# Kernel optimization log

Measured on AMD Instinct MI355X. Metric: run time of the kernel, lower is better.

## Reference

```python
import jax, jax.numpy as jnp
import numpy as np

N_ITEMS = 100001  # n_items + 1 (padding idx 0)
D = 128           # item_embedding_dim == hidden_size
P = 3             # purposes
S, B = 100, 256   # seq_len, batch
TAU = 0.1
EPS = 0.01


def setup_inputs() -> dict:
    key = jax.random.key(0)
    ks = jax.random.split(key, 6)
    std = 1.0 / np.sqrt(D)
    seq = jax.random.randint(ks[0], (S, B), 0, N_ITEMS)          # [S, B] item ids
    lens = jax.random.randint(ks[1], (B,), 1, S + 1)             # valid lengths in [1, S]
    emb_table = jax.random.uniform(ks[2], (N_ITEMS, D), minval=-std, maxval=std, dtype=jnp.float32)
    purpose_table = jax.random.uniform(ks[3], (P, D), minval=-std, maxval=std, dtype=jnp.float32)
    x2h_w = jax.random.uniform(ks[4], (P, 3 * D, D), minval=-std, maxval=std, dtype=jnp.float32)  # 3 cells
    h2h_w = jax.random.uniform(ks[5], (P, 3 * D, D), minval=-std, maxval=std, dtype=jnp.float32)
    return {"seq": seq, "lens": lens, "emb_table": emb_table,
            "purpose_table": purpose_table, "x2h_w": x2h_w, "h2h_w": h2h_w}


def _psru_cell(x, h, concen, Wx, Wh):
    # x: [B,D], h: [B,D], concen: [B], Wx/Wh: [3D, D]
    gx = x @ Wx.T                              # [B, 3D]
    gh = h @ Wh.T                              # [B, 3D]
    i_r, i_i, i_n = jnp.split(gx, 3, axis=1)
    h_r, h_i, h_n = jnp.split(gh, 3, axis=1)
    resetgate = jax.nn.sigmoid(i_r + h_r)
    inputgate = jax.nn.sigmoid(i_i + h_i)
    newgate = jnp.tanh(i_n + resetgate * h_n)
    multi = jnp.where(concen >= EPS, concen, 0.0)[:, None] * inputgate
    return h + multi * (newgate - h)


def reference(seq, lens, emb_table, purpose_table, x2h_w, h2h_w):
    # padding_idx = 0
    emb_table = emb_table.at[0].set(0.0)
    # concentration matrix: softmax over purposes of normalized-embedding similarity / tau
    item_n = emb_table / jnp.clip(jnp.linalg.norm(emb_table, axis=1, keepdims=True), 1e-12)
    attr_n = purpose_table / jnp.clip(jnp.linalg.norm(purpose_table, axis=1, keepdims=True), 1e-12)
    g = jax.nn.softmax((item_n @ attr_n.T) / TAU, axis=1)   # [V, P]  (exp/sum == softmax)
    g = g.at[0].set(0.0)

    embs = emb_table[seq]        # [S, B, D]
    g_seq = g[seq]               # [S, B, P]

    h0 = jnp.zeros((P, B, D), emb_table.dtype)

    def step(h, xs):
        x, gq = xs  # x: [B,D], gq: [B,P]
        h_new = jnp.stack([_psru_cell(x, h[p], gq[:, p], x2h_w[p], h2h_w[p]) for p in range(P)])
        return h_new, h_new

    _, hs = jax.lax.scan(step, h0, (embs, g_seq))            # hs: [S, P, B, D]

    # select hidden at last valid step per example: outs[lens-1, arange(B)]
    h_last = hs[lens - 1, :, jnp.arange(B), :]               # [B, P, D]

    # delta_c[b,v] = sum_p g[v,p] * <h_last[b,p], item_n[v]>  (== original VC_cand * item_embs sum)
    logits = sum((h_last[:, p, :] @ item_n.T) * g[None, :, p] for p in range(P))  # [B, V]
    return jax.nn.sigmoid(logits)
```

## Files before the change

kernel.cpp:

```cpp
#include <hip/hip_runtime.h>
#include <hip/hip_bf16.h>
#include <math.h>

#define N_ITEMS 100001
#define DIM 128
#define NP 3
#define SEQ 100
#define NB 256
#define G3 384
#define TAU 0.1f
#define EPS_C 0.01f

#define OFF_G     0
#define OFF_C     300016
#define OFF_WXT   600032
#define OFF_WHT   747488
#define OFF_HLAST 894944
#define OFF_GX    993248
#define WS_FLOATS_PATHA (993248 + 29491200)

typedef float f32x4 __attribute__((ext_vector_type(4)));
typedef short s16x8 __attribute__((ext_vector_type(8)));
typedef unsigned int u32x4 __attribute__((ext_vector_type(4)));
typedef _Float16 f16x8 __attribute__((ext_vector_type(8)));
typedef __fp16 hf16x2 __attribute__((ext_vector_type(2)));

__device__ __forceinline__ float sigmoidf_fast(float x) {
    return __builtin_amdgcn_rcpf(1.f + __builtin_amdgcn_exp2f(-1.4426950408889634f * x));
}
__device__ __forceinline__ float tanhf_fast(float x) {
    return 1.f - 2.f * __builtin_amdgcn_rcpf(1.f + __builtin_amdgcn_exp2f(2.8853900817779268f * x));
}
__device__ __forceinline__ unsigned short f2bf(float x) {
    union { float f; unsigned u; } v; v.f = x;
    unsigned r = v.u + 0x7fffu + ((v.u >> 16) & 1u);
    return (unsigned short)(r >> 16);
}
__device__ __forceinline__ float bf2f(unsigned short h) {
    union { unsigned u; float f; } v; v.u = ((unsigned)h) << 16;
    return v.f;
}
__device__ __forceinline__ unsigned cvt_pk_bf16(float a, float b) {
    unsigned r;
    asm("v_cvt_pk_bf16_f32 %0, %1, %2" : "=v"(r) : "v"(a), "v"(b));
    return r;
}
__device__ __forceinline__ f32x4 mfma16(s16x8 a, s16x8 b, f32x4 c) {
    return __builtin_amdgcn_mfma_f32_16x16x32_f16(
        __builtin_bit_cast(f16x8, a), __builtin_bit_cast(f16x8, b), c, 0, 0, 0);
}

__global__ void k_prep_w(const float* __restrict__ x2h, const float* __restrict__ h2h,
                         float* __restrict__ wxT, float* __restrict__ whT) {
    int idx = blockIdx.x * 256 + threadIdx.x;
    if (idx >= NP * DIM * G3) return;
    int j = idx % G3;
    int k = (idx / G3) % DIM;
    int p = idx / (G3 * DIM);
    wxT[idx] = x2h[((size_t)p * G3 + j) * DIM + k];
    whT[idx] = h2h[((size_t)p * G3 + j) * DIM + k];
}

__global__ __launch_bounds__(256) void k_prep_wA(const float* __restrict__ x2h,
                                                 const float* __restrict__ h2h,
                                                 short* __restrict__ wxA_hi,
                                                 short* __restrict__ wxA_lo,
                                                 short* __restrict__ whA_hi,
                                                 short* __restrict__ whA_lo) {
    int e = blockIdx.x * 256 + threadIdx.x;
    if (e >= 2 * NP * 24 * 4 * 64) return;
    int which = (e >= NP * 24 * 4 * 64);
    int f = which ? e - NP * 24 * 4 * 64 : e;
    const float* tab = which ? h2h : x2h;
    short* dh = which ? whA_hi : wxA_hi;
    short* dl = which ? whA_lo : wxA_lo;
    int lane = f & 63;
    int ks = (f >> 6) & 3;
    int mt = (f >> 8) % 24;
    int p  = f / 6144;
    int j = mt * 16 + (lane & 15);
    int d = ks * 32 + (lane >> 4) * 8;
    const float* src = tab + ((size_t)p * G3 + j) * DIM + d;
    short hi[8], lo[8];
    if (which) {
#pragma unroll
        for (int u = 0; u < 8; ++u) {
            float x = src[u];
            _Float16 hf = (_Float16)x;
            _Float16 lf = (_Float16)((x - (float)hf) * 2048.f);
            hi[u] = __builtin_bit_cast(short, hf);
            lo[u] = __builtin_bit_cast(short, lf);
        }
    } else {
#pragma unroll
        for (int u = 0; u < 8; ++u) {
            float x = src[u];
            unsigned short h = f2bf(x);
            hi[u] = (short)h;
            lo[u] = (short)f2bf(x - bf2f(h));
        }
    }
    *(s16x8*)(dh + (size_t)f * 8) = *(const s16x8*)hi;
    *(s16x8*)(dl + (size_t)f * 8) = *(const s16x8*)lo;
}

__global__ __launch_bounds__(256) void k_gc(const float* __restrict__ emb,
                                            const float* __restrict__ pt,
                                            float* __restrict__ g, float* __restrict__ c) {
    __shared__ float pt_l[G3];
    __shared__ float ainv[NP];
    int tid = threadIdx.x;
    for (int u = tid; u < G3; u += 256) pt_l[u] = pt[u];
    __syncthreads();
    if (tid < NP) {
        float ss = 0.f;
        for (int k = 0; k < DIM; ++k) { float v = pt_l[tid * DIM + k]; ss += v * v; }
        ainv[tid] = 1.f / fmaxf(sqrtf(ss), 1e-12f);
    }
    __syncthreads();
    int lane = tid & 63, wv = tid >> 6;
    for (int it = 0; it < 8; ++it) {
        int i = blockIdx.x * 32 + wv * 8 + it;
        if (i >= N_ITEMS) continue;
        float a = emb[(size_t)i * DIM + lane];
        float b = emb[(size_t)i * DIM + 64 + lane];
        float ss = a * a + b * b;
        float d0 = a * pt_l[lane]       + b * pt_l[64 + lane];
        float d1 = a * pt_l[128 + lane] + b * pt_l[192 + lane];
        float d2 = a * pt_l[256 + lane] + b * pt_l[320 + lane];
        for (int off = 32; off > 0; off >>= 1) {
            ss += __shfl_down(ss, off);
            d0 += __shfl_down(d0, off);
            d1 += __shfl_down(d1, off);
            d2 += __shfl_down(d2, off);
        }
        if (lane == 0) {
            if (i == 0) {
                g[0] = 0.f; g[1] = 0.f; g[2] = 0.f;
                c[0] = 0.f; c[1] = 0.f; c[2] = 0.f;
            } else {
                float inv = 1.f / fmaxf(sqrtf(ss), 1e-12f);
                float l0 = d0 * ainv[0] * inv * (1.f / TAU);
                float l1 = d1 * ainv[1] * inv * (1.f / TAU);
                float l2 = d2 * ainv[2] * inv * (1.f / TAU);
                float m = fmaxf(l0, fmaxf(l1, l2));
                float e0 = expf(l0 - m), e1 = expf(l1 - m), e2 = expf(l2 - m);
                float is = 1.f / (e0 + e1 + e2);
                float g0 = e0 * is, g1 = e1 * is, g2 = e2 * is;
                g[(size_t)i * 3 + 0] = g0; g[(size_t)i * 3 + 1] = g1; g[(size_t)i * 3 + 2] = g2;
                c[(size_t)i * 3 + 0] = g0 * inv; c[(size_t)i * 3 + 1] = g1 * inv; c[(size_t)i * 3 + 2] = g2 * inv;
            }
        }
    }
}

__global__ __launch_bounds__(512, 2) void k_gx_mfma(const int* __restrict__ seq,
                                                    const float* __restrict__ emb,
                                                    const short* __restrict__ wxA_hi,
                                                    const short* __restrict__ wxA_lo,
                                                    float* __restrict__ gx) {
    int bid = blockIdx.x;
    int t  = bid >> 4;
    int b0 = (bid & 15) * 16;
    int tid = threadIdx.x;
    int lane = tid & 63;
    int w = tid >> 6;
    int n = lane & 15;
    int q = lane >> 4;

    __shared__ int idx_l[16];
    __shared__ __align__(16) unsigned short xH[2048];
    __shared__ __align__(16) unsigned short xL[2048];

    if (tid < 16) idx_l[tid] = seq[t * NB + b0 + tid];
    __syncthreads();

    {
        int tk = tid >> 5, s = tid & 31;
        float4 v = *(const float4*)(emb + (size_t)idx_l[tk] * DIM + s * 4);
        int k = s * 4;
        int ks = k >> 5, km = k & 31;
        int ln = (km >> 3) * 16 + tk;
        int j0 = km & 7;
        int o = ks * 512 + ln * 8 + j0;
        float xv[4] = {v.x, v.y, v.z, v.w};
        unsigned short sh[4], sl[4];
#pragma unroll
        for (int r = 0; r < 4; ++r) {
            sh[r] = f2bf(xv[r]);
            sl[r] = f2bf(xv[r] - bf2f(sh[r]));
        }
        *(uint2*)(xH + o) = make_uint2((unsigned)sh[0] | ((unsigned)sh[1] << 16),
                                       (unsigned)sh[2] | ((unsigned)sh[3] << 16));
        *(uint2*)(xL + o) = make_uint2((unsigned)sl[0] | ((unsigned)sl[1] << 16),
                                       (unsigned)sl[2] | ((unsigned)sl[3] << 16));
    }
    __syncthreads();

    s16x8 bh[4], bl[4];
#pragma unroll
    for (int ks = 0; ks < 4; ++ks) {
        bh[ks] = ((const s16x8*)xH)[ks * 64 + lane];
        bl[ks] = ((const s16x8*)xL)[ks * 64 + lane];
    }

    float* gxt = gx + (size_t)(t * 3) * NB * G3;
#pragma unroll 3
    for (int ji = 0; ji < 9; ++ji) {
        int pid = w + ji * 8;
        int p = pid / 24, mt = pid % 24;
        f32x4 acc = {0.f, 0.f, 0.f, 0.f};
#pragma unroll
        for (int ks = 0; ks < 4; ++ks) {
            size_t ao = ((((size_t)p * 24 + mt) * 4 + ks) * 64 + lane) * 8;
            s16x8 ah = *(const s16x8*)(wxA_hi + ao);
            s16x8 al = *(const s16x8*)(wxA_lo + ao);
            acc = __builtin_amdgcn_mfma_f32_16x16x32_bf16(ah, bl[ks], acc, 0, 0, 0);
            acc = __builtin_amdgcn_mfma_f32_16x16x32_bf16(al, bh[ks], acc, 0, 0, 0);
            acc = __builtin_amdgcn_mfma_f32_16x16x32_bf16(ah, bh[ks], acc, 0, 0, 0);
        }
        float* o = gxt + ((size_t)p * NB + b0 + n) * G3 + mt * 16 + q * 4;
        *(float4*)o = make_float4(acc[0], acc[1], acc[2], acc[3]);
    }
}

__global__ __launch_bounds__(512, 2) void k_rnn3(const int* __restrict__ seq,
                                                 const int* __restrict__ lens,
                                                 const float* __restrict__ g,
                                                 const short* __restrict__ whA_hi,
                                                 const float* __restrict__ gx,
                                                 float* __restrict__ hlast) {
    int bid = blockIdx.x;
    int p  = bid / 16;
    int b0 = (bid % 16) * 16;
    int tid = threadIdx.x;
    int lane = tid & 63;
    int w = tid >> 6;
    int n = lane & 15;
    int q = lane >> 4;
    int d0 = w * 16 + q * 4;

    __shared__ __align__(16) unsigned short hH[2 * 2048];
    __shared__ __align__(16) unsigned short hL[2 * 2048];
    __shared__ float conc_s[SEQ * 16];

    for (int u = tid; u < 2048; u += 512) { hH[u] = 0; hL[u] = 0; }

    for (int e = tid; e < SEQ * 16; e += 512) {
        int t = e >> 4, b = e & 15;
        int ix = seq[t * NB + b0 + b];
        float cc = g[(size_t)ix * 3 + p];
        conc_s[e] = (cc >= EPS_C) ? cc : 0.f;
    }

    s16x8 whF[3][4];
    int mts0 = w, mts1 = 8 + w, mts2 = 16 + w;
#pragma unroll
    for (int ks = 0; ks < 4; ++ks) {
        size_t o0 = ((((size_t)p * 24 + mts0) * 4 + ks) * 64 + lane) * 8;
        size_t o1 = ((((size_t)p * 24 + mts1) * 4 + ks) * 64 + lane) * 8;
        size_t o2 = ((((size_t)p * 24 + mts2) * 4 + ks) * 64 + lane) * 8;
        whF[0][ks] = *(const s16x8*)(whA_hi + o0);
        whF[1][ks] = *(const s16x8*)(whA_hi + o1);
        whF[2][ks] = *(const s16x8*)(whA_hi + o2);
    }

    int len_n = lens[b0 + n];
    float h0 = 0.f, h1 = 0.f, h2 = 0.f, h3 = 0.f;

    int wks = d0 >> 5;
    int km  = d0 & 31;
    int rl  = (km >> 3) * 16 + n;
    int jj0 = km & 7;
    int widx = wks * 512 + rl * 8 + jj0;

    const float* gxbase = gx + ((size_t)p * NB + (b0 + n)) * G3 + d0;
    const size_t tstride = (size_t)3 * NB * G3;

    f32x4 pgr = *(const f32x4*)(gxbase);
    f32x4 pgi = *(const f32x4*)(gxbase + DIM);
    f32x4 pgn = *(const f32x4*)(gxbase + 2 * DIM);

    __syncthreads();

    const float SC = 4.8828125e-4f;

    int cur = 0;
    for (int t = 0; t < SEQ; ++t) {
        f32x4 grv = pgr, giv = pgi, gnv = pgn;
        int tn = (t + 1 < SEQ) ? (t + 1) : t;
        const float* gp = gxbase + (size_t)tn * tstride;
        pgr = *(const f32x4*)(gp);
        pgi = *(const f32x4*)(gp + DIM);
        pgn = *(const f32x4*)(gp + 2 * DIM);

        float cc = conc_s[t * 16 + n];

        const s16x8* bhp = (const s16x8*)hH + cur * 256 + lane;
        const s16x8* blp = (const s16x8*)hL + cur * 256 + lane;
        s16x8 bh0 = bhp[0],   bh1 = bhp[64],  bh2 = bhp[128], bh3 = bhp[192];
        s16x8 bl0 = blp[0],   bl1 = blp[64],  bl2 = blp[128], bl3 = blp[192];

        f32x4 aA0 = grv, aB0 = {0.f,0.f,0.f,0.f};
        aA0 = mfma16(whF[0][0], bh0, aA0);  aB0 = mfma16(whF[0][0], bl0, aB0);
        aA0 = mfma16(whF[0][1], bh1, aA0);  aB0 = mfma16(whF[0][1], bl1, aB0);
        aA0 = mfma16(whF[0][2], bh2, aA0);  aB0 = mfma16(whF[0][2], bl2, aB0);
        aA0 = mfma16(whF[0][3], bh3, aA0);  aB0 = mfma16(whF[0][3], bl3, aB0);
        __builtin_amdgcn_sched_barrier(0);
        float rr0 = sigmoidf_fast(fmaf(aB0[0], SC, aA0[0]));
        float rr1 = sigmoidf_fast(fmaf(aB0[1], SC, aA0[1]));
        float rr2 = sigmoidf_fast(fmaf(aB0[2], SC, aA0[2]));
        float rr3 = sigmoidf_fast(fmaf(aB0[3], SC, aA0[3]));
        __builtin_amdgcn_sched_barrier(0);
        f32x4 aA1 = giv, aB1 = {0.f,0.f,0.f,0.f};
        aA1 = mfma16(whF[1][0], bh0, aA1);  aB1 = mfma16(whF[1][0], bl0, aB1);
        aA1 = mfma16(whF[1][1], bh1, aA1);  aB1 = mfma16(whF[1][1], bl1, aB1);
        aA1 = mfma16(whF[1][2], bh2, aA1);  aB1 = mfma16(whF[1][2], bl2, aB1);
        aA1 = mfma16(whF[1][3], bh3, aA1);  aB1 = mfma16(whF[1][3], bl3, aB1);
        __builtin_amdgcn_sched_barrier(0);
        float m20 = cc * sigmoidf_fast(fmaf(aB1[0], SC, aA1[0]));
        float m21 = cc * sigmoidf_fast(fmaf(aB1[1], SC, aA1[1]));
        float m22 = cc * sigmoidf_fast(fmaf(aB1[2], SC, aA1[2]));
        float m23 = cc * sigmoidf_fast(fmaf(aB1[3], SC, aA1[3]));
        __builtin_amdgcn_sched_barrier(0);
        f32x4 aA2 = {0.f,0.f,0.f,0.f}, aB2 = {0.f,0.f,0.f,0.f};
        aA2 = mfma16(whF[2][0], bh0, aA2);  aB2 = mfma16(whF[2][0], bl0, aB2);
        aA2 = mfma16(whF[2][1], bh1, aA2);  aB2 = mfma16(whF[2][1], bl1, aB2);
        aA2 = mfma16(whF[2][2], bh2, aA2);  aB2 = mfma16(whF[2][2], bl2, aB2);
        aA2 = mfma16(whF[2][3], bh3, aA2);  aB2 = mfma16(whF[2][3], bl3, aB2);
        __builtin_amdgcn_sched_barrier(0);
        float hn0 = fmaf(aB2[0], SC, aA2[0]);
        float hn1 = fmaf(aB2[1], SC, aA2[1]);
        float hn2 = fmaf(aB2[2], SC, aA2[2]);
        float hn3 = fmaf(aB2[3], SC, aA2[3]);
        float ng0 = tanhf_fast(fmaf(rr0, hn0, gnv[0]));
        float ng1 = tanhf_fast(fmaf(rr1, hn1, gnv[1]));
        float ng2 = tanhf_fast(fmaf(rr2, hn2, gnv[2]));
        float ng3 = tanhf_fast(fmaf(rr3, hn3, gnv[3]));
        float hnew0 = fmaf(m20, ng0 - h0, h0);
        float hnew1 = fmaf(m21, ng1 - h1, h1);
        float hnew2 = fmaf(m22, ng2 - h2, h2);
        float hnew3 = fmaf(m23, ng3 - h3, h3);
        h0 = hnew0; h1 = hnew1; h2 = hnew2; h3 = hnew3;

        if (t == len_n - 1) {
            float* hp = hlast + (size_t)(b0 + n) * G3 + p * DIM + d0;
            *(float4*)hp = make_float4(h0, h1, h2, h3);
        }

        hf16x2 c01 = __builtin_amdgcn_cvt_pkrtz(hnew0, hnew1);
        hf16x2 c23 = __builtin_amdgcn_cvt_pkrtz(hnew2, hnew3);
        float e0 = (hnew0 - (float)c01[0]) * 2048.f;
        float e1 = (hnew1 - (float)c01[1]) * 2048.f;
        float e2 = (hnew2 - (float)c23[0]) * 2048.f;
        float e3 = (hnew3 - (float)c23[1]) * 2048.f;
        hf16x2 d01 = __builtin_amdgcn_cvt_pkrtz(e0, e1);
        hf16x2 d23 = __builtin_amdgcn_cvt_pkrtz(e2, e3);
        int wb = (cur ^ 1) * 2048 + widx;
        *(uint2*)(hH + wb) = make_uint2(__builtin_bit_cast(unsigned, c01),
                                        __builtin_bit_cast(unsigned, c23));
        *(uint2*)(hL + wb) = make_uint2(__builtin_bit_cast(unsigned, d01),
                                        __builtin_bit_cast(unsigned, d23));

        asm volatile("s_waitcnt lgkmcnt(0)" ::: "memory");
        __builtin_amdgcn_sched_barrier(0);
        __builtin_amdgcn_s_barrier();
        __builtin_amdgcn_sched_barrier(0);
        cur ^= 1;
    }
}

__global__ __launch_bounds__(384) void k_rnn(const int* __restrict__ seq,
                                             const int* __restrict__ lens,
                                             const float* __restrict__ emb,
                                             const float* __restrict__ g,
                                             const float* __restrict__ wxT,
                                             const float* __restrict__ whT,
                                             float* __restrict__ hlast) {
    int bid = blockIdx.x;
    int b0 = (bid & 63) * 4;
    int p = bid >> 6;
    __shared__ __align__(16) float h_l[DIM * 4];
    __shared__ __align__(16) float x_l[DIM * 4];
    __shared__ __align__(16) float sx_l[G3 * 4];
    __shared__ __align__(16) float sh_l[G3 * 4];
    __shared__ float conc_l[4];
    __shared__ int idx_l[4];
    __shared__ int len_l[4];
    int tid = threadIdx.x;
    if (tid < 4) len_l[tid] = lens[b0 + tid];
    for (int u = tid; u < DIM * 4; u += 384) h_l[u] = 0.f;
    __syncthreads();
    const float* wh = whT + (size_t)p * (DIM * G3);
    const float* wx = wxT + (size_t)p * (DIM * G3);
    for (int t = 0; t < SEQ; ++t) {
        if (tid < 4) {
            int ix = seq[t * NB + b0 + tid];
            idx_l[tid] = ix;
            conc_l[tid] = g[(size_t)ix * 3 + p];
        }
        __syncthreads();
        for (int u = tid; u < DIM * 4; u += 384) {
            int bc = u >> 7, k = u & 127;
            x_l[k * 4 + bc] = emb[(size_t)idx_l[bc] * DIM + k];
        }
        __syncthreads();
        int j = tid;
        float ax0 = 0.f, ax1 = 0.f, ax2 = 0.f, ax3 = 0.f;
#pragma unroll 4
        for (int k = 0; k < DIM; ++k) {
            float wv = wx[(size_t)k * G3 + j];
            float4 xv = *(const float4*)(x_l + k * 4);
            ax0 += wv * xv.x; ax1 += wv * xv.y; ax2 += wv * xv.z; ax3 += wv * xv.w;
        }
        float ah0 = 0.f, ah1 = 0.f, ah2 = 0.f, ah3 = 0.f;
#pragma unroll 4
        for (int k = 0; k < DIM; ++k) {
            float wv = wh[(size_t)k * G3 + j];
            float4 hv = *(const float4*)(h_l + k * 4);
            ah0 += wv * hv.x; ah1 += wv * hv.y; ah2 += wv * hv.z; ah3 += wv * hv.w;
        }
        *(float4*)(sx_l + j * 4) = make_float4(ax0, ax1, ax2, ax3);
        *(float4*)(sh_l + j * 4) = make_float4(ah0, ah1, ah2, ah3);
        __syncthreads();
        for (int u = tid; u < DIM * 4; u += 384) {
            int bc = u & 3, d = u >> 2;
            float sr = sx_l[d * 4 + bc] + sh_l[d * 4 + bc];
            float si = sx_l[(DIM + d) * 4 + bc] + sh_l[(DIM + d) * 4 + bc];
            float xn = sx_l[(2 * DIM + d) * 4 + bc];
            float hn = sh_l[(2 * DIM + d) * 4 + bc];
            float r  = sigmoidf_fast(sr);
            float ig = sigmoidf_fast(si);
            float ng = tanhf_fast(xn + r * hn);
            float h  = h_l[d * 4 + bc];
            float cc = conc_l[bc];
            float multi = (cc >= EPS_C ? cc : 0.f) * ig;
            float hnew = h + multi * (ng - h);
            h_l[d * 4 + bc] = hnew;
            if (t == len_l[bc] - 1)
                hlast[(size_t)(b0 + bc) * G3 + p * DIM + d] = hnew;
        }
        __syncthreads();
    }
}

__global__ __launch_bounds__(256) void k_prep_h(const float* __restrict__ hlast,
                                                short* __restrict__ hl_hi) {
    int e = blockIdx.x * 256 + threadIdx.x;
    int b = e / G3;
    int k = e % G3;
    float x = hlast[e];
    _Float16 hf = (_Float16)x;
    int off = (k >> 5) * 8192 + b * 32 + ((k >> 3) & 3) * 8 + (k & 7);
    hl_hi[off] = __builtin_bit_cast(short, hf);
}

__global__ __launch_bounds__(256) void k_logits_mfma(const float* __restrict__ emb,
                                                     const float* __restrict__ c,
                                                     const short* __restrict__ hl_hi,
                                                     float* __restrict__ out) {
    int i0 = blockIdx.x * 64;
    int tid = threadIdx.x;
    int w = tid >> 6;
    int lane = tid & 63;
    int n = lane & 15;
    int q = lane >> 4;

    __shared__ __align__(16) float embs[64 * 132];

    for (int u = tid; u < 64 * 32; u += 256) {
        int i = u >> 5;
        int s = u & 31;
        int gi = i0 + i;
        float4 v = make_float4(0.f, 0.f, 0.f, 0.f);
        if (gi < N_ITEMS) v = *(const float4*)(emb + (size_t)gi * DIM + s * 4);
        *(float4*)(embs + i * 132 + s * 4) = v;
    }

    float cv[4][3];
#pragma unroll
    for (int is = 0; is < 4; ++is) {
        int gi = i0 + is * 16 + n;
#pragma unroll
        for (int p = 0; p < 3; ++p)
            cv[is][p] = (gi < N_ITEMS) ? c[(size_t)gi * 3 + p] : 0.f;
    }
    __syncthreads();

    f32x4 acc[4][4];
#pragma unroll
    for (int bs = 0; bs < 4; ++bs)
#pragma unroll
        for (int is = 0; is < 4; ++is)
            acc[bs][is] = (f32x4){0.f, 0.f, 0.f, 0.f};

    for (int ks = 0; ks < 12; ++ks) {
        int p = ks >> 2;
        int d0 = (ks & 3) * 32;
        int abase = ks * 8192 + (w * 64 + n) * 32 + q * 8;
        s16x8 ah[4];
#pragma unroll
        for (int bs = 0; bs < 4; ++bs)
            ah[bs] = *(const s16x8*)(hl_hi + abase + bs * 512);
#pragma unroll
        for (int is = 0; is < 4; ++is) {
            const float* src = embs + (is * 16 + n) * 132 + d0 + q * 8;
            float x[8];
            *(float4*)(x)     = *(const float4*)(src);
            *(float4*)(x + 4) = *(const float4*)(src + 4);
            float sc = cv[is][p];
            union { hf16x2 h[4]; s16x8 s; } bf_;
#pragma unroll
            for (int jp = 0; jp < 4; ++jp)
                bf_.h[jp] = __builtin_amdgcn_cvt_pkrtz(x[2 * jp] * sc, x[2 * jp + 1] * sc);
            s16x8 bv = bf_.s;
#pragma unroll
            for (int bs = 0; bs < 4; ++bs)
                acc[bs][is] = mfma16(ah[bs], bv, acc[bs][is]);
        }
    }

#pragma unroll
    for (int is = 0; is < 4; ++is) {
        int gi = i0 + is * 16 + n;
        if (gi >= N_ITEMS) continue;
#pragma unroll
        for (int bs = 0; bs < 4; ++bs) {
            int brow = w * 64 + bs * 16 + q * 4;
#pragma unroll
            for (int r = 0; r < 4; ++r)
                out[(size_t)(brow + r) * N_ITEMS + gi] = sigmoidf_fast(acc[bs][is][r]);
        }
    }
}

extern "C" void kernel_launch(void* const* d_in, const int* in_sizes, int n_in,
                              void* d_out, int out_size, void* d_ws, size_t ws_size,
                              hipStream_t stream) {
    const int*   seq  = (const int*)d_in[0];
    const int*   lens = (const int*)d_in[1];
    const float* emb  = (const float*)d_in[2];
    const float* pt   = (const float*)d_in[3];
    const float* x2h  = (const float*)d_in[4];
    const float* h2h  = (const float*)d_in[5];
    float* out = (float*)d_out;
    float* ws  = (float*)d_ws;

    float* g     = ws + OFF_G;
    float* c     = ws + OFF_C;
    float* wxT   = ws + OFF_WXT;
    float* whT   = ws + OFF_WHT;
    float* hlast = ws + OFF_HLAST;
    float* gxbuf = ws + OFF_GX;
    short* wxA_hi = (short*)(ws + OFF_WXT);
    short* wxA_lo = wxA_hi + 147456;
    short* whA_hi = (short*)(ws + OFF_WHT);
    short* whA_lo = whA_hi + 147456;
    short* hl_hi = (short*)(ws + OFF_GX);

    int useGx = (ws_size >= (size_t)WS_FLOATS_PATHA * 4) ? 1 : 0;

    k_gc<<<3126, 256, 0, stream>>>(emb, pt, g, c);
    if (useGx) {
        k_prep_wA<<<144, 256, 0, stream>>>(x2h, h2h, wxA_hi, wxA_lo, whA_hi, whA_lo);
        k_gx_mfma<<<1600, 512, 0, stream>>>(seq, emb, wxA_hi, wxA_lo, gxbuf);
        k_rnn3<<<48, 512, 0, stream>>>(seq, lens, g, whA_hi, gxbuf, hlast);
    } else {
        k_prep_w<<<576, 256, 0, stream>>>(x2h, h2h, wxT, whT);
        k_rnn<<<192, 384, 0, stream>>>(seq, lens, emb, g, wxT, whT, hlast);
    }
    k_prep_h<<<384, 256, 0, stream>>>(hlast, hl_hi);
    k_logits_mfma<<<1563, 256, 0, stream>>>(emb, c, hl_hi, out);
}
```

Baseline: 390.4 us.

## Use single fp16 MFMA for input projection and merge RNN blocks to 1024 threads

The input-gate projection drops its three-pass bf16 hi/lo split and does one fp16 MFMA per k-step, with both the weights and the embedding converted to fp16. The recurrent kernel now runs 24 blocks of 1024 threads, each covering two 16-row batch tiles that share the per-purpose weight loads. The first change cuts MFMA work and global loads in k_gx_mfma but lowers accuracy. The second halves the block count and changes how the serial recurrence occupies the chip, which may lengthen each step because the block barrier now spans more waves.

After: 427.0 us. +9.4%, slower.

```diff
diff --git a/kernel.cpp b/kernel.cpp
--- a/kernel.cpp
+++ b/kernel.cpp
@@ -39,11 +39,6 @@
 __device__ __forceinline__ float bf2f(unsigned short h) {
     union { unsigned u; float f; } v; v.u = ((unsigned)h) << 16;
     return v.f;
-}
-__device__ __forceinline__ unsigned cvt_pk_bf16(float a, float b) {
-    unsigned r;
-    asm("v_cvt_pk_bf16_f32 %0, %1, %2" : "=v"(r) : "v"(a), "v"(b));
-    return r;
 }
 __device__ __forceinline__ f32x4 mfma16(s16x8 a, s16x8 b, f32x4 c) {
     return __builtin_amdgcn_mfma_f32_16x16x32_f16(
@@ -82,23 +77,13 @@
     int d = ks * 32 + (lane >> 4) * 8;
     const float* src = tab + ((size_t)p * G3 + j) * DIM + d;
     short hi[8], lo[8];
-    if (which) {
-#pragma unroll
-        for (int u = 0; u < 8; ++u) {
-            float x = src[u];
-            _Float16 hf = (_Float16)x;
-            _Float16 lf = (_Float16)((x - (float)hf) * 2048.f);
-            hi[u] = __builtin_bit_cast(short, hf);
-            lo[u] = __builtin_bit_cast(short, lf);
-        }
-    } else {
-#pragma unroll
-        for (int u = 0; u < 8; ++u) {
-            float x = src[u];
-            unsigned short h = f2bf(x);
-            hi[u] = (short)h;
-            lo[u] = (short)f2bf(x - bf2f(h));
-        }
+#pragma unroll
+    for (int u = 0; u < 8; ++u) {
+        float x = src[u];
+        _Float16 hf = (_Float16)x;
+        _Float16 lf = (_Float16)((x - (float)hf) * 2048.f);
+        hi[u] = __builtin_bit_cast(short, hf);
+        lo[u] = __builtin_bit_cast(short, lf);
     }
     *(s16x8*)(dh + (size_t)f * 8) = *(const s16x8*)hi;
     *(s16x8*)(dl + (size_t)f * 8) = *(const s16x8*)lo;
@@ -156,8 +141,7 @@
 
 __global__ __launch_bounds__(512, 2) void k_gx_mfma(const int* __restrict__ seq,
                                                     const float* __restrict__ emb,
-                                                    const short* __restrict__ wxA_hi,
-                                                    const short* __restrict__ wxA_lo,
+                                                    const short* __restrict__ wxA,
                                                     float* __restrict__ gx) {
     int bid = blockIdx.x;
     int t  = bid >> 4;
@@ -169,8 +153,7 @@
     int q = lane >> 4;
 
     __shared__ int idx_l[16];
-    __shared__ __align__(16) unsigned short xH[2048];
-    __shared__ __align__(16) unsigned short xL[2048];
+    __shared__ __align__(16) unsigned short xF[2048];
 
     if (tid < 16) idx_l[tid] = seq[t * NB + b0 + tid];
     __syncthreads();
@@ -183,26 +166,17 @@
         int ln = (km >> 3) * 16 + tk;
         int j0 = km & 7;
         int o = ks * 512 + ln * 8 + j0;
-        float xv[4] = {v.x, v.y, v.z, v.w};
-        unsigned short sh[4], sl[4];
-#pragma unroll
-        for (int r = 0; r < 4; ++r) {
-            sh[r] = f2bf(xv[r]);
-            sl[r] = f2bf(xv[r] - bf2f(sh[r]));
-        }
-        *(uint2*)(xH + o) = make_uint2((unsigned)sh[0] | ((unsigned)sh[1] << 16),
-                                       (unsigned)sh[2] | ((unsigned)sh[3] << 16));
-        *(uint2*)(xL + o) = make_uint2((unsigned)sl[0] | ((unsigned)sl[1] << 16),
-                                       (unsigned)sl[2] | ((unsigned)sl[3] << 16));
-    }
-    __syncthreads();
-
-    s16x8 bh[4], bl[4];
-#pragma unroll
-    for (int ks = 0; ks < 4; ++ks) {
-        bh[ks] = ((const s16x8*)xH)[ks * 64 + lane];
-        bl[ks] = ((const s16x8*)xL)[ks * 64 + lane];
-    }
+        hf16x2 a01 = __builtin_amdgcn_cvt_pkrtz(v.x, v.y);
+        hf16x2 a23 = __builtin_amdgcn_cvt_pkrtz(v.z, v.w);
+        *(uint2*)(xF + o) = make_uint2(__builtin_bit_cast(unsigned, a01),
+                                       __builtin_bit_cast(unsigned, a23));
+    }
+    __syncthreads();
+
+    s16x8 bf[4];
+#pragma unroll
+    for (int ks = 0; ks < 4; ++ks)
+        bf[ks] = ((const s16x8*)xF)[ks * 64 + lane];
 
     float* gxt = gx + (size_t)(t * 3) * NB * G3;
 #pragma unroll 3
@@ -213,42 +187,42 @@
 #pragma unroll
         for (int ks = 0; ks < 4; ++ks) {
             size_t ao = ((((size_t)p * 24 + mt) * 4 + ks) * 64 + lane) * 8;
-            s16x8 ah = *(const s16x8*)(wxA_hi + ao);
-            s16x8 al = *(const s16x8*)(wxA_lo + ao);
-            acc = __builtin_amdgcn_mfma_f32_16x16x32_bf16(ah, bl[ks], acc, 0, 0, 0);
-            acc = __builtin_amdgcn_mfma_f32_16x16x32_bf16(al, bh[ks], acc, 0, 0, 0);
-            acc = __builtin_amdgcn_mfma_f32_16x16x32_bf16(ah, bh[ks], acc, 0, 0, 0);
+            s16x8 af = *(const s16x8*)(wxA + ao);
+            acc = mfma16(af, bf[ks], acc);
         }
         float* o = gxt + ((size_t)p * NB + b0 + n) * G3 + mt * 16 + q * 4;
         *(float4*)o = make_float4(acc[0], acc[1], acc[2], acc[3]);
     }
 }
 
-__global__ __launch_bounds__(512, 2) void k_rnn3(const int* __restrict__ seq,
-                                                 const int* __restrict__ lens,
-                                                 const float* __restrict__ g,
-                                                 const short* __restrict__ whA_hi,
-                                                 const float* __restrict__ gx,
-                                                 float* __restrict__ hlast) {
+__global__ __launch_bounds__(1024, 4) void k_rnn3(const int* __restrict__ seq,
+                                                  const int* __restrict__ lens,
+                                                  const float* __restrict__ g,
+                                                  const short* __restrict__ whA_hi,
+                                                  const float* __restrict__ gx,
+                                                  float* __restrict__ hlast) {
     int bid = blockIdx.x;
-    int p  = bid / 16;
-    int b0 = (bid % 16) * 16;
+    int p  = bid / 8;
+    int bg = bid % 8;
     int tid = threadIdx.x;
+    int tile2 = tid >> 9;
+    int tl  = tid & 511;
     int lane = tid & 63;
-    int w = tid >> 6;
+    int w = tl >> 6;
     int n = lane & 15;
     int q = lane >> 4;
     int d0 = w * 16 + q * 4;
-
-    __shared__ __align__(16) unsigned short hH[2 * 2048];
-    __shared__ __align__(16) unsigned short hL[2 * 2048];
-    __shared__ float conc_s[SEQ * 16];
-
-    for (int u = tid; u < 2048; u += 512) { hH[u] = 0; hL[u] = 0; }
-
-    for (int e = tid; e < SEQ * 16; e += 512) {
-        int t = e >> 4, b = e & 15;
-        int ix = seq[t * NB + b0 + b];
+    int b0 = bg * 32 + tile2 * 16;
+
+    __shared__ __align__(16) unsigned short hH[2 * 4096];
+    __shared__ __align__(16) unsigned short hL[2 * 4096];
+    __shared__ float conc_s[SEQ * 32];
+
+    for (int u = tid; u < 4096; u += 1024) { hH[u] = 0; hL[u] = 0; }
+
+    for (int e = tid; e < SEQ * 32; e += 1024) {
+        int t = e >> 5, b = e & 31;
+        int ix = seq[t * NB + bg * 32 + b];
         float cc = g[(size_t)ix * 3 + p];
         conc_s[e] = (cc >= EPS_C) ? cc : 0.f;
     }
@@ -294,10 +268,10 @@
         pgi = *(const f32x4*)(gp + DIM);
         pgn = *(const f32x4*)(gp + 2 * DIM);
 
-        float cc = conc_s[t * 16 + n];
-
-        const s16x8* bhp = (const s16x8*)hH + cur * 256 + lane;
-        const s16x8* blp = (const s16x8*)hL + cur * 256 + lane;
+        float cc = conc_s[t * 32 + tile2 * 16 + n];
+
+        const s16x8* bhp = (const s16x8*)hH + cur * 512 + tile2 * 256 + lane;
+        const s16x8* blp = (const s16x8*)hL + cur * 512 + tile2 * 256 + lane;
         s16x8 bh0 = bhp[0],   bh1 = bhp[64],  bh2 = bhp[128], bh3 = bhp[192];
         s16x8 bl0 = blp[0],   bl1 = blp[64],  bl2 = blp[128], bl3 = blp[192];
 
@@ -356,7 +330,7 @@
         float e3 = (hnew3 - (float)c23[1]) * 2048.f;
         hf16x2 d01 = __builtin_amdgcn_cvt_pkrtz(e0, e1);
         hf16x2 d23 = __builtin_amdgcn_cvt_pkrtz(e2, e3);
-        int wb = (cur ^ 1) * 2048 + widx;
+        int wb = (cur ^ 1) * 4096 + tile2 * 2048 + widx;
         *(uint2*)(hH + wb) = make_uint2(__builtin_bit_cast(unsigned, c01),
                                         __builtin_bit_cast(unsigned, c23));
         *(uint2*)(hL + wb) = make_uint2(__builtin_bit_cast(unsigned, d01),
@@ -563,8 +537,8 @@
     k_gc<<<3126, 256, 0, stream>>>(emb, pt, g, c);
     if (useGx) {
         k_prep_wA<<<144, 256, 0, stream>>>(x2h, h2h, wxA_hi, wxA_lo, whA_hi, whA_lo);
-        k_gx_mfma<<<1600, 512, 0, stream>>>(seq, emb, wxA_hi, wxA_lo, gxbuf);
-        k_rnn3<<<48, 512, 0, stream>>>(seq, lens, g, whA_hi, gxbuf, hlast);
+        k_gx_mfma<<<1600, 512, 0, stream>>>(seq, emb, wxA_hi, gxbuf);
+        k_rnn3<<<24, 1024, 0, stream>>>(seq, lens, g, whA_hi, gxbuf, hlast);
     } else {
         k_prep_w<<<576, 256, 0, stream>>>(x2h, h2h, wxT, whT);
         k_rnn<<<192, 384, 0, stream>>>(seq, lens, emb, g, wxT, whT, hlast);
```
